# Optimization experiments

Measured on AMD Instinct MI355X. Metric: run time of the kernel, lower is better.

The kernel has to match this reference:

```python
import jax, jax.numpy as jnp
import numpy as np

B, D, O = 32768, 512, 16          # batch, input_size, output_size
E, K, T = 16, 4, 3                # n_expert, top-k, n_task
H1, H2 = 16, 8                    # Expert hidden sizes (hard-coded in Expert)
SPARSE_COEF, OLMO_COEF, RZ_COEF = 0.01, 0.01, 0.001


def setup_inputs() -> dict:
    key = jax.random.key(0)
    ks = jax.random.split(key, 8)
    s = 0.05
    return {
        "x": jax.random.normal(ks[0], (B, D), jnp.float32),
        # per-task gate params (torch inits zeros; random here for a meaningful test)
        "w_gates": jax.random.normal(ks[1], (T, D, E), jnp.float32) * s,
        "b_gates": jnp.zeros((T, E), jnp.float32),
        # stacked expert MLP params: Linear(D,16)->ReLU->Linear(16,8)->ReLU->Linear(8,O)->ReLU
        "W1": jax.random.normal(ks[2], (E, D, H1), jnp.float32) * s,
        "b1": jnp.zeros((E, H1), jnp.float32),
        "W2": jax.random.normal(ks[3], (E, H1, H2), jnp.float32) * s,
        "b2": jnp.zeros((E, H2), jnp.float32),
        "W3": jax.random.normal(ks[4], (E, H2, O), jnp.float32) * s,
        "b3": jnp.zeros((E, O), jnp.float32),
    }


def cv_squared(v):
    # torch .var() is unbiased (ddof=1)
    eps = 1e-10
    return jnp.var(v, ddof=1) / (jnp.mean(v) ** 2 + eps)


def reference(x, w_gates, b_gates, W1, b1, W2, b2, W3, b3):
    Bn = x.shape[0]
    # router z loss uses raw input x (as in the source)
    rz_per_task = jnp.sum(jax.nn.logsumexp(x, axis=-1)) / Bn

    # All experts on all samples, vectorized over the expert axis.
    # (experts are identical across tasks, so compute once; gating makes it sparse)
    h1 = jax.nn.relu(jnp.einsum('bd,edh->ebh', x, W1) + b1[:, None, :])   # [E,B,16]
    h2 = jax.nn.relu(jnp.einsum('ebh,ehk->ebk', h1, W2) + b2[:, None, :])  # [E,B,8]
    eo = jax.nn.relu(jnp.einsum('ebk,eko->ebo', h2, W3) + b3[:, None, :])  # [E,B,O]

    row = jnp.arange(Bn)[:, None]
    ys = []
    lb_loss = jnp.float32(0.0)
    rz_loss = jnp.float32(0.0)
    for t in range(T):  # small fixed task loop
        logits = x @ w_gates[t] + b_gates[t]               # [B,E]
        top_vals, top_idx = jax.lax.top_k(logits, K)
        top_gates = jax.nn.softmax(top_vals, axis=1)
        gates = jnp.zeros_like(logits).at[row, top_idx].set(top_gates)  # [B,E]

        load = (gates > 0).sum(0).astype(jnp.float32)      # eval-mode load
        importance = gates.sum(0)
        sparse_lb = cv_squared(importance) + cv_squared(load)
        olmo_lb = E * jnp.sum(importance * (load / Bn))
        lb_loss = lb_loss + sparse_lb * SPARSE_COEF + olmo_lb * OLMO_COEF
        rz_loss = rz_loss + rz_per_task * RZ_COEF

        # combine: y[b] = sum_e gates[b,e] * expert_e(x[b])
        ys.append(jnp.einsum('be,ebo->bo', gates, eo))
    return (jnp.stack(ys), lb_loss, rz_loss)
```

## Files before the change

### kernel.cpp

```cpp
#include <hip/hip_runtime.h>
#include <hip/hip_bf16.h>

#define BSZ 32768
#define TT  3
#define OO  16

typedef __attribute__((ext_vector_type(8))) short bf16x8;
typedef __attribute__((ext_vector_type(4))) float f32x4;

__device__ __forceinline__ float bf2f(unsigned short u) {
  return __uint_as_float(((unsigned)u) << 16);
}
__device__ __forceinline__ unsigned short f2bf(float f) {
  unsigned u = __float_as_uint(f);
  u += 0x7fffu + ((u >> 16) & 1u);
  return (unsigned short)(u >> 16);
}
__device__ __forceinline__ unsigned pack2(unsigned short a, unsigned short b) {
  return (unsigned)a | ((unsigned)b << 16);
}

__global__ void k_prepw(const float* __restrict__ W1, const float* __restrict__ wg,
                        unsigned short* __restrict__ Wfh,
                        unsigned short* __restrict__ Wfl, float* __restrict__ acc) {
  if (blockIdx.x == 0 && threadIdx.x < 97) acc[threadIdx.x] = 0.f;
  for (int idx = blockIdx.x * 256 + threadIdx.x; idx < 20 * 16 * 64 * 8;
       idx += gridDim.x * 256) {
    const int nblk = idx >> 13, itg = (idx >> 9) & 15;
    const int lane = (idx >> 3) & 63, j = idx & 7;
    const int n = nblk * 16 + (lane & 15);
    const int k = itg * 32 + (lane >> 4) * 8 + j;
    float v = 0.f;
    if (n < 256) v = W1[(size_t)(n >> 4) * 8192 + k * 16 + (n & 15)];
    else if (n < 304) v = wg[(size_t)((n - 256) >> 4) * 8192 + k * 16 + ((n - 256) & 15)];
    const unsigned short hi = f2bf(v);
    Wfh[idx] = hi;
    Wfl[idx] = f2bf(v - bf2f(hi));
  }
}

struct FSmem {
  union {
    struct {
      unsigned short xh[4][4][64][8];
      unsigned short xl[4][4][64][8];
    } a;
    struct {
      unsigned short hd[16][264];
      float eoL[16][16][17];
      float gvL[64][12];
      int   giL[64][12];
      union {
        float lgs[64][52];
        struct { float W2t[2048], W3t[2048]; } t;
      } u2;
      float b2t[128], b3t[256];
      float impL[48], loadL[48];
      int   nresc, resc[192];
      double resL[16];
    } b;
  } u;
  float rzrow[64];
};

__global__ __launch_bounds__(512, 4) void k_fused(
    const float* __restrict__ x, const unsigned short* __restrict__ Wfh,
    const unsigned short* __restrict__ Wfl, const float* __restrict__ b1,
    const float* __restrict__ bg, const float* __restrict__ wg,
    const float* __restrict__ W2, const float* __restrict__ b2,
    const float* __restrict__ W3, const float* __restrict__ b3,
    float* __restrict__ out, float* __restrict__ acc_imp,
    float* __restrict__ acc_load, float* __restrict__ rz_acc) {
  __shared__ FSmem sm;
  const int tid = threadIdx.x;
  const int b0 = blockIdx.x * 64;
  const int w = tid >> 6, l = tid & 63;
  const int l15 = l & 15, quad = l >> 4;
  const int mh = w >> 2;
  const int cg = w & 3;
  const int srow = tid >> 3, skf = tid & 7;
  const int sm_abs = srow >> 4;
  const int slane = (srow & 15) + 16 * (skf >> 1);
  const int sj = (skf & 1) * 4;

  f32x4 acc[2][5];
#pragma unroll
  for (int m = 0; m < 2; m++)
#pragma unroll
    for (int c = 0; c < 5; c++) acc[m][c] = (f32x4){0.f, 0.f, 0.f, 0.f};
  float rzsum = 0.f;

  auto woffs = [&](int itg, int c) -> size_t {
    return ((size_t)(((cg * 5 + c) * 16 + itg) * 64 + l)) * 8;
  };

#pragma unroll 1
  for (int ch = 0; ch < 4; ++ch) {
    if (ch) __syncthreads();
    {
      float4 xv[4];
      const float* xp = &x[(size_t)(b0 + srow) * 512 + ch * 128 + skf * 4];
#pragma unroll
      for (int r = 0; r < 4; r++) xv[r] = *(const float4*)(xp + r * 32);
#pragma unroll
      for (int r = 0; r < 4; r++) {
        const float v0 = xv[r].x, v1 = xv[r].y, v2 = xv[r].z, v3 = xv[r].w;
        rzsum += __expf(v0) + __expf(v1) + __expf(v2) + __expf(v3);
        const unsigned short h0 = f2bf(v0), h1_ = f2bf(v1), h2_ = f2bf(v2), h3 = f2bf(v3);
        uint2 ph, pl;
        ph.x = pack2(h0, h1_); ph.y = pack2(h2_, h3);
        pl.x = pack2(f2bf(v0 - bf2f(h0)), f2bf(v1 - bf2f(h1_)));
        pl.y = pack2(f2bf(v2 - bf2f(h2_)), f2bf(v3 - bf2f(h3)));
        *(uint2*)&sm.u.a.xh[sm_abs][r][slane][sj] = ph;
        *(uint2*)&sm.u.a.xl[sm_abs][r][slane][sj] = pl;
      }
    }
    __syncthreads();

    bf16x8 bh = *(const bf16x8*)&Wfh[woffs(ch * 4, 0)];
    bf16x8 bl = *(const bf16x8*)&Wfl[woffs(ch * 4, 0)];
#pragma unroll
    for (int it = 0; it < 4; ++it) {
      bf16x8 ah[2], al[2];
#pragma unroll
      for (int m = 0; m < 2; m++) {
        ah[m] = *(const bf16x8*)&sm.u.a.xh[mh * 2 + m][it][l][0];
        al[m] = *(const bf16x8*)&sm.u.a.xl[mh * 2 + m][it][l][0];
      }
#pragma unroll
      for (int c = 0; c < 5; c++) {
        bf16x8 bhn = bh, bln = bl;
        if (!((it == 3) && (c == 4))) {
          const int nit = (c == 4) ? it + 1 : it;
          const int nc  = (c == 4) ? 0 : c + 1;
          const size_t o = woffs(ch * 4 + nit, nc);
          bhn = *(const bf16x8*)&Wfh[o];
          bln = *(const bf16x8*)&Wfl[o];
        }
#pragma unroll
        for (int m = 0; m < 2; m++) {
          acc[m][c] = __builtin_amdgcn_mfma_f32_16x16x32_bf16(ah[m], bh, acc[m][c], 0, 0, 0);
          acc[m][c] = __builtin_amdgcn_mfma_f32_16x16x32_bf16(al[m], bh, acc[m][c], 0, 0, 0);
          acc[m][c] = __builtin_amdgcn_mfma_f32_16x16x32_bf16(ah[m], bl, acc[m][c], 0, 0, 0);
        }
        bh = bhn; bl = bln;
      }
    }
  }

  rzsum += __shfl_xor(rzsum, 1);
  rzsum += __shfl_xor(rzsum, 2);
  rzsum += __shfl_xor(rzsum, 4);
  if (skf == 0) sm.rzrow[srow] = rzsum;
  __syncthreads();

  if (tid < 64) {
    float vv = __logf(sm.rzrow[tid]);
#pragma unroll
    for (int off = 32; off; off >>= 1) vv += __shfl_xor(vv, off);
    if (tid == 0) atomicAdd(rz_acc, vv);
  }
  if (cg == 3) {
#pragma unroll
    for (int c = 1; c < 4; c++) {
      const int cc = 16 * c + l15 - 16;
#pragma unroll
      for (int m = 0; m < 2; m++)
#pragma unroll
        for (int reg = 0; reg < 4; reg++) {
          const int row = 32 * mh + 16 * m + quad * 4 + reg;
          sm.u.b.u2.lgs[row][cc] = acc[m][c][reg] + bg[cc];
        }
    }
  }
  if (tid < 48) { sm.u.b.impL[tid] = 0.f; sm.u.b.loadL[tid] = 0.f; }
  if (tid == 0) sm.u.b.nresc = 0;
  __syncthreads();

  if (tid < 192) {
    const int r = tid & 63, tk = tid >> 6;
    float v[16];
#pragma unroll
    for (int e = 0; e < 16; e++) v[e] = sm.u.b.u2.lgs[r][tk * 16 + e];
    unsigned used = 0;
    int idx[5]; float val[5];
#pragma unroll
    for (int p = 0; p < 5; p++) {
      float best = -INFINITY; int bi = 0;
#pragma unroll
      for (int e = 0; e < 16; e++) {
        const float ve = ((used >> e) & 1u) ? -INFINITY : v[e];
        if (ve > best) { best = ve; bi = e; }
      }
      idx[p] = bi; val[p] = best; used |= 1u << bi;
    }
    if (val[3] - val[4] < 3e-3f) {
      const int s = atomicAdd(&sm.u.b.nresc, 1);
      sm.u.b.resc[s] = (r << 2) | tk;
    }
    const float m = val[0];
    float ex[4], sum = 0.f;
#pragma unroll
    for (int p = 0; p < 4; p++) { ex[p] = __expf(val[p] - m); sum += ex[p]; }
#pragma unroll
    for (int p = 0; p < 4; p++) {
      const float g = ex[p] / sum;
      sm.u.b.gvL[r][tk * 4 + p] = g;
      sm.u.b.giL[r][tk * 4 + p] = idx[p];
      atomicAdd(&sm.u.b.impL[tk * 16 + idx[p]], g);
      atomicAdd(&sm.u.b.loadL[tk * 16 + idx[p]], 1.f);
    }
  }
  __syncthreads();

  const int nr = sm.u.b.nresc;
  for (int i = 0; i < nr; i++) {
    const int st = sm.u.b.resc[i];
    const int r = st >> 2, tk = st & 3;
    if (tid < 256) {
      const int e = tid >> 4, part = tid & 15;
      const float* xr2 = &x[(size_t)(b0 + r) * 512];
      const float* wgc = &wg[(size_t)tk * 8192 + e];
      double a = 0.0;
      for (int d = part * 32; d < part * 32 + 32; d++)
        a += (double)xr2[d] * (double)wgc[(size_t)d * 16];
#pragma unroll
      for (int off = 1; off < 16; off <<= 1) a += __shfl_xor(a, off);
      if (part == 0) sm.u.b.resL[e] = a + (double)bg[tk * 16 + e];
    }
    __syncthreads();
    if (tid == 0) {
      for (int p = 0; p < 4; p++) {
        sm.u.b.impL[tk * 16 + sm.u.b.giL[r][tk * 4 + p]] -= sm.u.b.gvL[r][tk * 4 + p];
        sm.u.b.loadL[tk * 16 + sm.u.b.giL[r][tk * 4 + p]] -= 1.f;
      }
      unsigned used = 0;
      int idx[4]; float val[4];
      for (int p = 0; p < 4; p++) {
        double best = -1e300; int bi = 0;
        for (int e2 = 0; e2 < 16; e2++) {
          if ((used >> e2) & 1u) continue;
          const double ve = sm.u.b.resL[e2];
          if (ve > best) { best = ve; bi = e2; }
        }
        idx[p] = bi; val[p] = (float)best; used |= 1u << bi;
      }
      const float m = val[0];
      float ex[4], sum = 0.f;
      for (int p = 0; p < 4; p++) { ex[p] = __expf(val[p] - m); sum += ex[p]; }
      for (int p = 0; p < 4; p++) {
        const float g = ex[p] / sum;
        sm.u.b.gvL[r][tk * 4 + p] = g;
        sm.u.b.giL[r][tk * 4 + p] = idx[p];
        sm.u.b.impL[tk * 16 + idx[p]] += g;
        sm.u.b.loadL[tk * 16 + idx[p]] += 1.f;
      }
    }
    __syncthreads();
  }
  if (tid < 48) {
    atomicAdd(&acc_imp[tid], sm.u.b.impL[tid]);
    atomicAdd(&acc_load[tid], sm.u.b.loadL[tid]);
  }

  for (int d = tid; d < 2048; d += 512) {
    sm.u.b.u2.t.W2t[(d & 127) * 16 + (d >> 7)] = W2[d];
    sm.u.b.u2.t.W3t[(d & 127) * 16 + (d >> 7)] = W3[d];
  }
  if (tid < 128) sm.u.b.b2t[(tid & 7) * 16 + (tid >> 3)] = b2[tid];
  if (tid < 256) sm.u.b.b3t[(tid & 15) * 16 + (tid >> 4)] = b3[tid];
  __syncthreads();

#pragma unroll
  for (int ch = 0; ch < 4; ++ch) {
    if (mh == (ch >> 1)) {
      const int m = ch & 1;
#pragma unroll
      for (int c = 0; c < 5; c++) {
        const int col = 80 * cg + 16 * c + l15;
        if (col < 256) {
#pragma unroll
          for (int reg = 0; reg < 4; reg++)
            sm.u.b.hd[quad * 4 + reg][col] = f2bf(fmaxf(acc[m][c][reg] + b1[col], 0.f));
        }
      }
    }
    __syncthreads();
    if (tid < 256) {
      const int e = tid & 15, sr = tid >> 4;
      float h1v[16];
#pragma unroll
      for (int q = 0; q < 4; q++) {
        const ushort4 uu = *(const ushort4*)&sm.u.b.hd[sr][e * 16 + q * 4];
        h1v[q * 4 + 0] = bf2f(uu.x);
        h1v[q * 4 + 1] = bf2f(uu.y);
        h1v[q * 4 + 2] = bf2f(uu.z);
        h1v[q * 4 + 3] = bf2f(uu.w);
      }
      float h2v[8];
#pragma unroll
      for (int j = 0; j < 8; j++) {
        float a = sm.u.b.b2t[j * 16 + e];
#pragma unroll
        for (int k = 0; k < 16; k++) a += h1v[k] * sm.u.b.u2.t.W2t[(k * 8 + j) * 16 + e];
        h2v[j] = fmaxf(a, 0.f);
      }
#pragma unroll
      for (int o = 0; o < 16; o++) {
        float a = sm.u.b.b3t[o * 16 + e];
#pragma unroll
        for (int j = 0; j < 8; j++) a += h2v[j] * sm.u.b.u2.t.W3t[(j * 16 + o) * 16 + e];
        sm.u.b.eoL[sr][e][o] = fmaxf(a, 0.f);
      }
    }
    __syncthreads();
    if (tid < 256) {
      const int o = tid & 15, sr = tid >> 4;
      const int rl = ch * 16 + sr;
#pragma unroll
      for (int tk = 0; tk < TT; tk++) {
        float y = 0.f;
#pragma unroll
        for (int p = 0; p < 4; p++)
          y += sm.u.b.gvL[rl][tk * 4 + p] * sm.u.b.eoL[sr][sm.u.b.giL[rl][tk * 4 + p]][o];
        out[((size_t)tk * BSZ + b0 + rl) * OO + o] = y;
      }
    }
    __syncthreads();
  }
}

__global__ void k_final(const float* __restrict__ acc_imp,
                        const float* __restrict__ acc_load,
                        const float* __restrict__ rz_acc,
                        float* __restrict__ out_tail) {
  if (threadIdx.x == 0 && blockIdx.x == 0) {
    double lb = 0.0;
    for (int t = 0; t < TT; t++) {
      const float* imp = &acc_imp[t * 16];
      const float* ld = &acc_load[t * 16];
      double si = 0, sl = 0, dot = 0;
      for (int e2 = 0; e2 < 16; e2++) {
        si += imp[e2]; sl += ld[e2]; dot += (double)imp[e2] * ld[e2];
      }
      const double mi = si / 16.0, ml = sl / 16.0;
      double vi = 0, vl = 0;
      for (int e2 = 0; e2 < 16; e2++) {
        const double di = imp[e2] - mi, dl = ld[e2] - ml;
        vi += di * di; vl += dl * dl;
      }
      vi /= 15.0; vl /= 15.0;
      lb += (vi / (mi * mi + 1e-10) + vl / (ml * ml + 1e-10)) * 0.01
          + 16.0 * dot / (double)BSZ * 0.01;
    }
    out_tail[0] = (float)lb;
    out_tail[1] = (float)(3.0 * (rz_acc[0] / (double)BSZ) * 0.001);
  }
}

extern "C" void kernel_launch(void* const* d_in, const int* in_sizes, int n_in,
                              void* d_out, int out_size, void* d_ws, size_t ws_size,
                              hipStream_t stream) {
  const float* x  = (const float*)d_in[0];
  const float* wg = (const float*)d_in[1];
  const float* bg = (const float*)d_in[2];
  const float* W1 = (const float*)d_in[3];
  const float* b1 = (const float*)d_in[4];
  const float* W2 = (const float*)d_in[5];
  const float* b2 = (const float*)d_in[6];
  const float* W3 = (const float*)d_in[7];
  const float* b3 = (const float*)d_in[8];
  float* out = (float*)d_out;

  char* wsb = (char*)d_ws;
  unsigned short* Wfh = (unsigned short*)wsb;
  unsigned short* Wfl = (unsigned short*)(wsb + 327680);
  float* acc = (float*)(wsb + 655360);

  k_prepw<<<dim3(640), dim3(256), 0, stream>>>(W1, wg, Wfh, Wfl, acc);
  k_fused<<<dim3(BSZ / 64), dim3(512), 0, stream>>>(
      x, Wfh, Wfl, b1, bg, wg, W2, b2, W3, b3, out, acc, acc + 48, acc + 96);
  k_final<<<dim3(1), dim3(64), 0, stream>>>(acc, acc + 48, acc + 96,
                                            out + (size_t)TT * BSZ * OO);
}
```

Baseline: 236.8 us.

## Move expert layers 2-3 to MFMA, double block rows, fold final reduction into kernel

Expert layers 2 and 3 now run as block-diagonal bf16 hi/lo MFMA products instead of scalar FMA loops in LDS. To feed them, W2 and W3 are pre-split into MFMA fragments in the prep kernel. Each block now handles 128 rows with a 4-deep weight register prefetch ring, and the next x chunk is loaded while the current one is being multiplied. The separate final kernel is replaced by a last-block-done atomic counter, which removes one launch. The grid shrinks to 256 blocks at occupancy 2, so there are fewer waves to hide latency, and register pressure rises with 4x5 accumulators.

```diff
diff --git a/kernel.cpp b/kernel.cpp
--- a/kernel.cpp
+++ b/kernel.cpp
@@ -20,168 +20,217 @@
   return (unsigned)a | ((unsigned)b << 16);
 }
 
-__global__ void k_prepw(const float* __restrict__ W1, const float* __restrict__ wg,
-                        unsigned short* __restrict__ Wfh,
-                        unsigned short* __restrict__ Wfl, float* __restrict__ acc) {
-  if (blockIdx.x == 0 && threadIdx.x < 97) acc[threadIdx.x] = 0.f;
-  for (int idx = blockIdx.x * 256 + threadIdx.x; idx < 20 * 16 * 64 * 8;
-       idx += gridDim.x * 256) {
-    const int nblk = idx >> 13, itg = (idx >> 9) & 15;
-    const int lane = (idx >> 3) & 63, j = idx & 7;
+__global__ void k_prep(const float* __restrict__ W1, const float* __restrict__ wg,
+                       const float* __restrict__ W2, const float* __restrict__ W3,
+                       unsigned short* __restrict__ Wfh, unsigned short* __restrict__ Wfl,
+                       unsigned short* __restrict__ W2fh, unsigned short* __restrict__ W2fl,
+                       unsigned short* __restrict__ W3fh, unsigned short* __restrict__ W3fl,
+                       float* __restrict__ acc) {
+  const int idx = blockIdx.x * 256 + threadIdx.x;
+  if (blockIdx.x == 0 && threadIdx.x < 98) acc[threadIdx.x] = 0.f;
+  if (idx < 163840) {
+    const int nblk = idx >> 13, itg = (idx >> 9) & 15, lane = (idx >> 3) & 63, j = idx & 7;
     const int n = nblk * 16 + (lane & 15);
     const int k = itg * 32 + (lane >> 4) * 8 + j;
     float v = 0.f;
     if (n < 256) v = W1[(size_t)(n >> 4) * 8192 + k * 16 + (n & 15)];
     else if (n < 304) v = wg[(size_t)((n - 256) >> 4) * 8192 + k * 16 + ((n - 256) & 15)];
     const unsigned short hi = f2bf(v);
-    Wfh[idx] = hi;
-    Wfl[idx] = f2bf(v - bf2f(hi));
+    Wfh[idx] = hi; Wfl[idx] = f2bf(v - bf2f(hi));
+  } else if (idx < 163840 + 4096) {
+    const int i = idx - 163840;
+    const int nt = i >> 9, l = (i >> 3) & 63, j = i & 7;
+    const int cc = l & 15, kw = ((l >> 4) << 3) + j;
+    float v = 0.f;
+    if ((kw >> 4) == (cc >> 3)) v = W2[(2 * nt + (cc >> 3)) * 128 + (kw & 15) * 8 + (cc & 7)];
+    const unsigned short hi = f2bf(v);
+    W2fh[i] = hi; W2fl[i] = f2bf(v - bf2f(hi));
+  } else if (idx < 163840 + 4096 + 8192) {
+    const int i = idx - 163840 - 4096;
+    const int e = i >> 9, l = (i >> 3) & 63, j = i & 7;
+    const int cc = l & 15, kw = ((l >> 4) << 3) + j;
+    float v = 0.f;
+    if ((kw >> 3) == (e & 3)) v = W3[e * 128 + (kw & 7) * 16 + cc];
+    const unsigned short hi = f2bf(v);
+    W3fh[i] = hi; W3fl[i] = f2bf(v - bf2f(hi));
   }
 }
 
 struct FSmem {
   union {
     struct {
-      unsigned short xh[4][4][64][8];
-      unsigned short xl[4][4][64][8];
+      unsigned short xh[8][4][66][8];
+      unsigned short xl[8][4][66][8];
     } a;
     struct {
-      unsigned short hd[16][264];
-      float eoL[16][16][17];
-      float gvL[64][12];
-      int   giL[64][12];
       union {
-        float lgs[64][52];
-        struct { float W2t[2048], W3t[2048]; } t;
-      } u2;
-      float b2t[128], b3t[256];
+        unsigned short h1A[8][8][64][8];
+        float eoC[32][264];
+      } r2;
+      unsigned short h2Ah[8][4][64][8];
+      union {
+        float lgs[128][52];
+        unsigned short h2Al[8][4][64][8];
+      } r1;
+      float gvL[128][12];
+      int   giL[128][12];
       float impL[48], loadL[48];
-      int   nresc, resc[192];
+      int   nresc, resc[384];
       double resL[16];
     } b;
   } u;
-  float rzrow[64];
+  float rzrow[128];
 };
 
-__global__ __launch_bounds__(512, 4) void k_fused(
+__global__ __launch_bounds__(512, 2) void k_fused(
     const float* __restrict__ x, const unsigned short* __restrict__ Wfh,
-    const unsigned short* __restrict__ Wfl, const float* __restrict__ b1,
+    const unsigned short* __restrict__ Wfl, const unsigned short* __restrict__ W2fh,
+    const unsigned short* __restrict__ W2fl, const unsigned short* __restrict__ W3fh,
+    const unsigned short* __restrict__ W3fl, const float* __restrict__ b1,
     const float* __restrict__ bg, const float* __restrict__ wg,
-    const float* __restrict__ W2, const float* __restrict__ b2,
-    const float* __restrict__ W3, const float* __restrict__ b3,
-    float* __restrict__ out, float* __restrict__ acc_imp,
-    float* __restrict__ acc_load, float* __restrict__ rz_acc) {
+    const float* __restrict__ b2, const float* __restrict__ b3,
+    float* __restrict__ out, float* __restrict__ accg) {
   __shared__ FSmem sm;
+  __shared__ int islast;
   const int tid = threadIdx.x;
-  const int b0 = blockIdx.x * 64;
+  const int b0 = blockIdx.x * 128;
   const int w = tid >> 6, l = tid & 63;
   const int l15 = l & 15, quad = l >> 4;
   const int mh = w >> 2;
   const int cg = w & 3;
-  const int srow = tid >> 3, skf = tid & 7;
-  const int sm_abs = srow >> 4;
-  const int slane = (srow & 15) + 16 * (skf >> 1);
-  const int sj = (skf & 1) * 4;
-
-  f32x4 acc[2][5];
-#pragma unroll
-  for (int m = 0; m < 2; m++)
+  const int srow = tid >> 2, skf = tid & 3;
+
+  float* acc_imp = accg;
+  float* acc_load = accg + 48;
+  float* rz_acc = accg + 96;
+
+  f32x4 acc[4][5];
+#pragma unroll
+  for (int m = 0; m < 4; m++)
 #pragma unroll
     for (int c = 0; c < 5; c++) acc[m][c] = (f32x4){0.f, 0.f, 0.f, 0.f};
   float rzsum = 0.f;
 
-  auto woffs = [&](int itg, int c) -> size_t {
-    return ((size_t)(((cg * 5 + c) * 16 + itg) * 64 + l)) * 8;
+  float4 xv[8];
+  auto load_x = [&](int ch) {
+    const float* xp = &x[(size_t)(b0 + srow) * 512 + ch * 128 + skf * 32];
+#pragma unroll
+    for (int r = 0; r < 8; ++r) xv[r] = *(const float4*)(xp + r * 4);
   };
+  auto cvt_store = [&]() {
+#pragma unroll
+    for (int q = 0; q < 4; ++q) {
+      const float v[8] = {xv[2 * q].x, xv[2 * q].y, xv[2 * q].z, xv[2 * q].w,
+                          xv[2 * q + 1].x, xv[2 * q + 1].y, xv[2 * q + 1].z, xv[2 * q + 1].w};
+#pragma unroll
+      for (int j = 0; j < 8; j++) rzsum += __expf(v[j]);
+      unsigned short hh[8], ll[8];
+#pragma unroll
+      for (int j = 0; j < 8; j++) {
+        hh[j] = f2bf(v[j]);
+        ll[j] = f2bf(v[j] - bf2f(hh[j]));
+      }
+      uint4 ph, pl;
+      ph.x = pack2(hh[0], hh[1]); ph.y = pack2(hh[2], hh[3]);
+      ph.z = pack2(hh[4], hh[5]); ph.w = pack2(hh[6], hh[7]);
+      pl.x = pack2(ll[0], ll[1]); pl.y = pack2(ll[2], ll[3]);
+      pl.z = pack2(ll[4], ll[5]); pl.w = pack2(ll[6], ll[7]);
+      const int lane = (srow & 15) + 16 * q;
+      *(uint4*)&sm.u.a.xh[srow >> 4][skf][lane][0] = ph;
+      *(uint4*)&sm.u.a.xl[srow >> 4][skf][lane][0] = pl;
+    }
+  };
+
+  bf16x8 rbh[4], rbl[4];
+#pragma unroll
+  for (int s = 0; s < 4; ++s) {
+    const size_t o = ((size_t)((cg * 5 + s) * 16) * 64 + l) * 8;
+    rbh[s] = *(const bf16x8*)&Wfh[o];
+    rbl[s] = *(const bf16x8*)&Wfl[o];
+  }
+  load_x(0);
 
 #pragma unroll 1
   for (int ch = 0; ch < 4; ++ch) {
     if (ch) __syncthreads();
-    {
-      float4 xv[4];
-      const float* xp = &x[(size_t)(b0 + srow) * 512 + ch * 128 + skf * 4];
-#pragma unroll
-      for (int r = 0; r < 4; r++) xv[r] = *(const float4*)(xp + r * 32);
-#pragma unroll
-      for (int r = 0; r < 4; r++) {
-        const float v0 = xv[r].x, v1 = xv[r].y, v2 = xv[r].z, v3 = xv[r].w;
-        rzsum += __expf(v0) + __expf(v1) + __expf(v2) + __expf(v3);
-        const unsigned short h0 = f2bf(v0), h1_ = f2bf(v1), h2_ = f2bf(v2), h3 = f2bf(v3);
-        uint2 ph, pl;
-        ph.x = pack2(h0, h1_); ph.y = pack2(h2_, h3);
-        pl.x = pack2(f2bf(v0 - bf2f(h0)), f2bf(v1 - bf2f(h1_)));
-        pl.y = pack2(f2bf(v2 - bf2f(h2_)), f2bf(v3 - bf2f(h3)));
-        *(uint2*)&sm.u.a.xh[sm_abs][r][slane][sj] = ph;
-        *(uint2*)&sm.u.a.xl[sm_abs][r][slane][sj] = pl;
-      }
-    }
+    cvt_store();
     __syncthreads();
-
-    bf16x8 bh = *(const bf16x8*)&Wfh[woffs(ch * 4, 0)];
-    bf16x8 bl = *(const bf16x8*)&Wfl[woffs(ch * 4, 0)];
+    if (ch < 3) load_x(ch + 1);
 #pragma unroll
     for (int it = 0; it < 4; ++it) {
-      bf16x8 ah[2], al[2];
-#pragma unroll
-      for (int m = 0; m < 2; m++) {
-        ah[m] = *(const bf16x8*)&sm.u.a.xh[mh * 2 + m][it][l][0];
-        al[m] = *(const bf16x8*)&sm.u.a.xl[mh * 2 + m][it][l][0];
-      }
-#pragma unroll
-      for (int c = 0; c < 5; c++) {
-        bf16x8 bhn = bh, bln = bl;
-        if (!((it == 3) && (c == 4))) {
-          const int nit = (c == 4) ? it + 1 : it;
-          const int nc  = (c == 4) ? 0 : c + 1;
-          const size_t o = woffs(ch * 4 + nit, nc);
-          bhn = *(const bf16x8*)&Wfh[o];
-          bln = *(const bf16x8*)&Wfl[o];
-        }
-#pragma unroll
-        for (int m = 0; m < 2; m++) {
+      bf16x8 ah[4], al[4];
+#pragma unroll
+      for (int m = 0; m < 4; m++) {
+        ah[m] = *(const bf16x8*)&sm.u.a.xh[mh * 4 + m][it][l][0];
+        al[m] = *(const bf16x8*)&sm.u.a.xl[mh * 4 + m][it][l][0];
+      }
+#pragma unroll
+      for (int c = 0; c < 5; ++c) {
+        const int j = it * 5 + c;
+        bf16x8 bh = rbh[j & 3], bl = rbl[j & 3];
+        const int jn = j + 4;
+        if (ch * 20 + jn < 80) {
+          const int itgn = ch * 4 + jn / 5;
+          const int cn = jn % 5;
+          const size_t o = ((size_t)((cg * 5 + cn) * 16 + itgn) * 64 + l) * 8;
+          rbh[j & 3] = *(const bf16x8*)&Wfh[o];
+          rbl[j & 3] = *(const bf16x8*)&Wfl[o];
+        }
+#pragma unroll
+        for (int m = 0; m < 4; m++)
           acc[m][c] = __builtin_amdgcn_mfma_f32_16x16x32_bf16(ah[m], bh, acc[m][c], 0, 0, 0);
+#pragma unroll
+        for (int m = 0; m < 4; m++)
           acc[m][c] = __builtin_amdgcn_mfma_f32_16x16x32_bf16(al[m], bh, acc[m][c], 0, 0, 0);
+#pragma unroll
+        for (int m = 0; m < 4; m++)
           acc[m][c] = __builtin_amdgcn_mfma_f32_16x16x32_bf16(ah[m], bl, acc[m][c], 0, 0, 0);
-        }
-        bh = bhn; bl = bln;
       }
     }
   }
 
   rzsum += __shfl_xor(rzsum, 1);
   rzsum += __shfl_xor(rzsum, 2);
-  rzsum += __shfl_xor(rzsum, 4);
   if (skf == 0) sm.rzrow[srow] = rzsum;
   __syncthreads();
-
-  if (tid < 64) {
+  if (tid < 128) {
     float vv = __logf(sm.rzrow[tid]);
 #pragma unroll
     for (int off = 32; off; off >>= 1) vv += __shfl_xor(vv, off);
-    if (tid == 0) atomicAdd(rz_acc, vv);
-  }
-  if (cg == 3) {
-#pragma unroll
-    for (int c = 1; c < 4; c++) {
-      const int cc = 16 * c + l15 - 16;
-#pragma unroll
-      for (int m = 0; m < 2; m++)
+    if ((tid & 63) == 0) atomicAdd(rz_acc, vv);
+  }
+
+#pragma unroll
+  for (int m = 0; m < 4; m++)
+#pragma unroll
+    for (int c = 0; c < 5; c++) {
+      const int col = cg * 80 + c * 16 + l15;
+      if (col < 256) {
+        const float bb = b1[col];
 #pragma unroll
         for (int reg = 0; reg < 4; reg++) {
-          const int row = 32 * mh + 16 * m + quad * 4 + reg;
-          sm.u.b.u2.lgs[row][cc] = acc[m][c][reg] + bg[cc];
-        }
-    }
-  }
+          const int ri = quad * 4 + reg;
+          sm.u.b.r2.h1A[mh * 4 + m][col >> 5][ri + 16 * ((col & 31) >> 3)][col & 7] =
+              f2bf(fmaxf(acc[m][c][reg] + bb, 0.f));
+        }
+      } else if (col < 304) {
+        const float bb = bg[col - 256];
+#pragma unroll
+        for (int reg = 0; reg < 4; reg++) {
+          const int row = (mh * 4 + m) * 16 + quad * 4 + reg;
+          sm.u.b.r1.lgs[row][col - 256] = acc[m][c][reg] + bb;
+        }
+      }
+    }
   if (tid < 48) { sm.u.b.impL[tid] = 0.f; sm.u.b.loadL[tid] = 0.f; }
   if (tid == 0) sm.u.b.nresc = 0;
   __syncthreads();
 
-  if (tid < 192) {
-    const int r = tid & 63, tk = tid >> 6;
+  if (tid < 384) {
+    const int r = tid & 127, tk = tid >> 7;
     float v[16];
 #pragma unroll
-    for (int e = 0; e < 16; e++) v[e] = sm.u.b.u2.lgs[r][tk * 16 + e];
+    for (int e = 0; e < 16; e++) v[e] = sm.u.b.r1.lgs[r][tk * 16 + e];
     unsigned used = 0;
     int idx[5]; float val[5];
 #pragma unroll
@@ -262,99 +311,110 @@
     atomicAdd(&acc_imp[tid], sm.u.b.impL[tid]);
     atomicAdd(&acc_load[tid], sm.u.b.loadL[tid]);
   }
-
-  for (int d = tid; d < 2048; d += 512) {
-    sm.u.b.u2.t.W2t[(d & 127) * 16 + (d >> 7)] = W2[d];
-    sm.u.b.u2.t.W3t[(d & 127) * 16 + (d >> 7)] = W3[d];
-  }
-  if (tid < 128) sm.u.b.b2t[(tid & 7) * 16 + (tid >> 3)] = b2[tid];
-  if (tid < 256) sm.u.b.b3t[(tid & 15) * 16 + (tid >> 4)] = b3[tid];
-  __syncthreads();
-
-#pragma unroll
-  for (int ch = 0; ch < 4; ++ch) {
-    if (mh == (ch >> 1)) {
-      const int m = ch & 1;
-#pragma unroll
-      for (int c = 0; c < 5; c++) {
-        const int col = 80 * cg + 16 * c + l15;
-        if (col < 256) {
+  __syncthreads();
+
+  {
+    const bf16x8 w2h = *(const bf16x8*)&W2fh[(size_t)(w * 64 + l) * 8];
+    const bf16x8 w2l = *(const bf16x8*)&W2fl[(size_t)(w * 64 + l) * 8];
+    const float b2v = b2[w * 16 + l15];
+    const int kit = w >> 1;
+    const int lane2b = 16 * (2 * (w & 1) + (l15 >> 3));
+    const int j2 = l15 & 7;
+#pragma unroll
+    for (int m = 0; m < 8; m++) {
+      const bf16x8 a = *(const bf16x8*)&sm.u.b.r2.h1A[m][w][l][0];
+      f32x4 a2 = __builtin_amdgcn_mfma_f32_16x16x32_bf16(a, w2h, (f32x4){0.f, 0.f, 0.f, 0.f}, 0, 0, 0);
+      a2 = __builtin_amdgcn_mfma_f32_16x16x32_bf16(a, w2l, a2, 0, 0, 0);
+#pragma unroll
+      for (int reg = 0; reg < 4; reg++) {
+        const float val = fmaxf(a2[reg] + b2v, 0.f);
+        const unsigned short hi = f2bf(val);
+        const int lane2 = (quad * 4 + reg) + lane2b;
+        sm.u.b.h2Ah[m][kit][lane2][j2] = hi;
+        sm.u.b.r1.h2Al[m][kit][lane2][j2] = f2bf(val - bf2f(hi));
+      }
+    }
+  }
+  __syncthreads();
+
+  {
+    bf16x8 w3h[2], w3l[2];
+    float b3v[2];
+#pragma unroll
+    for (int ee = 0; ee < 2; ee++) {
+      const int e = w + ee * 8;
+      w3h[ee] = *(const bf16x8*)&W3fh[(size_t)(e * 64 + l) * 8];
+      w3l[ee] = *(const bf16x8*)&W3fl[(size_t)(e * 64 + l) * 8];
+      b3v[ee] = b3[e * 16 + l15];
+    }
+#pragma unroll 1
+    for (int p = 0; p < 4; ++p) {
+#pragma unroll
+      for (int mm = 0; mm < 2; ++mm) {
+        const int m = p * 2 + mm;
+#pragma unroll
+        for (int ee = 0; ee < 2; ++ee) {
+          const int e = w + ee * 8;
+          const bf16x8 hh = *(const bf16x8*)&sm.u.b.h2Ah[m][e >> 2][l][0];
+          const bf16x8 hl = *(const bf16x8*)&sm.u.b.r1.h2Al[m][e >> 2][l][0];
+          f32x4 a3 = __builtin_amdgcn_mfma_f32_16x16x32_bf16(hh, w3h[ee], (f32x4){0.f, 0.f, 0.f, 0.f}, 0, 0, 0);
+          a3 = __builtin_amdgcn_mfma_f32_16x16x32_bf16(hl, w3h[ee], a3, 0, 0, 0);
+          a3 = __builtin_amdgcn_mfma_f32_16x16x32_bf16(hh, w3l[ee], a3, 0, 0, 0);
 #pragma unroll
           for (int reg = 0; reg < 4; reg++)
-            sm.u.b.hd[quad * 4 + reg][col] = f2bf(fmaxf(acc[m][c][reg] + b1[col], 0.f));
-        }
-      }
-    }
+            sm.u.b.r2.eoC[mm * 16 + quad * 4 + reg][e * 16 + l15] = fmaxf(a3[reg] + b3v[ee], 0.f);
+        }
+      }
+      __syncthreads();
+      {
+        const int row16 = tid >> 4, o = tid & 15;
+        const int r_abs = p * 32 + row16;
+#pragma unroll
+        for (int tk = 0; tk < TT; tk++) {
+          float y = 0.f;
+#pragma unroll
+          for (int pp = 0; pp < 4; pp++) {
+            const float g = sm.u.b.gvL[r_abs][tk * 4 + pp];
+            const int gi = sm.u.b.giL[r_abs][tk * 4 + pp];
+            y += g * sm.u.b.r2.eoC[row16][gi * 16 + o];
+          }
+          out[((size_t)tk * BSZ + b0 + r_abs) * OO + o] = y;
+        }
+      }
+      __syncthreads();
+    }
+  }
+
+  __threadfence();
+  if (tid == 0) islast = (atomicAdd((int*)(accg + 97), 1) == 255);
+  __syncthreads();
+  if (islast) {
+    float* fin = &sm.u.b.gvL[0][0];
+    if (tid < 97) fin[tid] = atomicAdd(&accg[tid], 0.f);
     __syncthreads();
-    if (tid < 256) {
-      const int e = tid & 15, sr = tid >> 4;
-      float h1v[16];
-#pragma unroll
-      for (int q = 0; q < 4; q++) {
-        const ushort4 uu = *(const ushort4*)&sm.u.b.hd[sr][e * 16 + q * 4];
-        h1v[q * 4 + 0] = bf2f(uu.x);
-        h1v[q * 4 + 1] = bf2f(uu.y);
-        h1v[q * 4 + 2] = bf2f(uu.z);
-        h1v[q * 4 + 3] = bf2f(uu.w);
-      }
-      float h2v[8];
-#pragma unroll
-      for (int j = 0; j < 8; j++) {
-        float a = sm.u.b.b2t[j * 16 + e];
-#pragma unroll
-        for (int k = 0; k < 16; k++) a += h1v[k] * sm.u.b.u2.t.W2t[(k * 8 + j) * 16 + e];
-        h2v[j] = fmaxf(a, 0.f);
-      }
-#pragma unroll
-      for (int o = 0; o < 16; o++) {
-        float a = sm.u.b.b3t[o * 16 + e];
-#pragma unroll
-        for (int j = 0; j < 8; j++) a += h2v[j] * sm.u.b.u2.t.W3t[(j * 16 + o) * 16 + e];
-        sm.u.b.eoL[sr][e][o] = fmaxf(a, 0.f);
-      }
-    }
-    __syncthreads();
-    if (tid < 256) {
-      const int o = tid & 15, sr = tid >> 4;
-      const int rl = ch * 16 + sr;
-#pragma unroll
-      for (int tk = 0; tk < TT; tk++) {
-        float y = 0.f;
-#pragma unroll
-        for (int p = 0; p < 4; p++)
-          y += sm.u.b.gvL[rl][tk * 4 + p] * sm.u.b.eoL[sr][sm.u.b.giL[rl][tk * 4 + p]][o];
-        out[((size_t)tk * BSZ + b0 + rl) * OO + o] = y;
-      }
-    }
-    __syncthreads();
-  }
-}
-
-__global__ void k_final(const float* __restrict__ acc_imp,
-                        const float* __restrict__ acc_load,
-                        const float* __restrict__ rz_acc,
-                        float* __restrict__ out_tail) {
-  if (threadIdx.x == 0 && blockIdx.x == 0) {
-    double lb = 0.0;
-    for (int t = 0; t < TT; t++) {
-      const float* imp = &acc_imp[t * 16];
-      const float* ld = &acc_load[t * 16];
-      double si = 0, sl = 0, dot = 0;
-      for (int e2 = 0; e2 < 16; e2++) {
-        si += imp[e2]; sl += ld[e2]; dot += (double)imp[e2] * ld[e2];
-      }
-      const double mi = si / 16.0, ml = sl / 16.0;
-      double vi = 0, vl = 0;
-      for (int e2 = 0; e2 < 16; e2++) {
-        const double di = imp[e2] - mi, dl = ld[e2] - ml;
-        vi += di * di; vl += dl * dl;
-      }
-      vi /= 15.0; vl /= 15.0;
-      lb += (vi / (mi * mi + 1e-10) + vl / (ml * ml + 1e-10)) * 0.01
-          + 16.0 * dot / (double)BSZ * 0.01;
-    }
-    out_tail[0] = (float)lb;
-    out_tail[1] = (float)(3.0 * (rz_acc[0] / (double)BSZ) * 0.001);
+    if (tid == 0) {
+      double lb = 0.0;
+      for (int t = 0; t < TT; t++) {
+        const float* imp = &fin[t * 16];
+        const float* ld = &fin[48 + t * 16];
+        double si = 0, sl = 0, dot = 0;
+        for (int e2 = 0; e2 < 16; e2++) {
+          si += imp[e2]; sl += ld[e2]; dot += (double)imp[e2] * ld[e2];
+        }
+        const double mi = si / 16.0, ml = sl / 16.0;
+        double vi = 0, vl = 0;
+        for (int e2 = 0; e2 < 16; e2++) {
+          const double di = imp[e2] - mi, dl = ld[e2] - ml;
+          vi += di * di; vl += dl * dl;
+        }
+        vi /= 15.0; vl /= 15.0;
+        lb += (vi / (mi * mi + 1e-10) + vl / (ml * ml + 1e-10)) * 0.01
+            + 16.0 * dot / (double)BSZ * 0.01;
+      }
+      float* out_tail = out + (size_t)TT * BSZ * OO;
+      out_tail[0] = (float)lb;
+      out_tail[1] = (float)(3.0 * ((double)fin[96] / (double)BSZ) * 0.001);
+    }
   }
 }
 
@@ -373,13 +433,16 @@
   float* out = (float*)d_out;
 
   char* wsb = (char*)d_ws;
-  unsigned short* Wfh = (unsigned short*)wsb;
-  unsigned short* Wfl = (unsigned short*)(wsb + 327680);
-  float* acc = (float*)(wsb + 655360);
-
-  k_prepw<<<dim3(640), dim3(256), 0, stream>>>(W1, wg, Wfh, Wfl, acc);
-  k_fused<<<dim3(BSZ / 64), dim3(512), 0, stream>>>(
-      x, Wfh, Wfl, b1, bg, wg, W2, b2, W3, b3, out, acc, acc + 48, acc + 96);
-  k_final<<<dim3(1), dim3(64), 0, stream>>>(acc, acc + 48, acc + 96,
-                                            out + (size_t)TT * BSZ * OO);
-}
+  unsigned short* Wfh  = (unsigned short*)wsb;
+  unsigned short* Wfl  = (unsigned short*)(wsb + 327680);
+  unsigned short* W2fh = (unsigned short*)(wsb + 655360);
+  unsigned short* W2fl = (unsigned short*)(wsb + 663552);
+  unsigned short* W3fh = (unsigned short*)(wsb + 671744);
+  unsigned short* W3fl = (unsigned short*)(wsb + 688128);
+  float* acc = (float*)(wsb + 704512);
+
+  k_prep<<<dim3(688), dim3(256), 0, stream>>>(W1, wg, W2, W3, Wfh, Wfl,
+                                              W2fh, W2fl, W3fh, W3fl, acc);
+  k_fused<<<dim3(256), dim3(512), 0, stream>>>(x, Wfh, Wfl, W2fh, W2fl, W3fh, W3fl,
+                                               b1, bg, wg, b2, b3, out, acc);
+}
```

Result: slower. 254.1 us (+7.3%).
